# Optimization experiments

Hardware: AMD Instinct MI355X
Metric: run time of the kernel (lower is better)

The kernel has to match this reference:

```python
import jax, jax.numpy as jnp
import numpy as np

B = 4096          # batch_size
D = 256           # embedding dim
N = 2 * B
TEMPERATURE = 0.5
GAMMA = 2.0
ALPHA = 0.25


def _negative_indices():
    # Static column indices of negatives per row: all columns except self (i)
    # and the positive partner ((i+B) mod N). Shape (N, N-2).
    idx = []
    for i in range(N):
        partner = (i + B) % N
        cols = [j for j in range(N) if j != i and j != partner]
        idx.append(cols)
    return np.asarray(idx, dtype=np.int32)

_NEG_IDX = jnp.asarray(_negative_indices())


def setup_inputs() -> dict:
    key = jax.random.key(0)
    kx, ky = jax.random.split(key)
    zx = jax.random.normal(kx, (B, D), dtype=jnp.float32)
    zy = jax.random.normal(ky, (B, D), dtype=jnp.float32)
    return {"zx": zx, "zy": zy}


def reference(zx, zy):
    z = jnp.concatenate([zx, zy], axis=0)                    # (N, D)
    zn = z / jnp.linalg.norm(z, axis=1, keepdims=True)       # cosine normalize
    sim = (zn @ zn.T) / TEMPERATURE                          # (N, N)

    sim_xy = jnp.diagonal(sim, offset=B)                     # (B,)
    sim_yx = jnp.diagonal(sim, offset=-B)                    # (B,)
    pos = jnp.concatenate([sim_xy, sim_yx])[:, None]         # (N, 1)
    neg = jnp.take_along_axis(sim, _NEG_IDX, axis=1)         # (N, N-2)

    logits = jnp.concatenate([pos, neg], axis=1)             # (N, N-1)
    # CE with label 0 for every row: -log_softmax(logits)[:, 0]
    ce = jax.nn.logsumexp(logits, axis=1) - logits[:, 0]
    pt = jnp.exp(-ce)
    focal = (1.0 - pt) ** GAMMA * ce
    return (ALPHA * focal).mean()
```

## Files before the change

kernel.cpp:

```cpp
#include <hip/hip_runtime.h>
#include <stdint.h>
#include <stddef.h>


typedef __attribute__((ext_vector_type(8))) short short8;
typedef __attribute__((ext_vector_type(4))) float f32x4;

#define NROWS 8192
#define DDIM 256
#define NTILES 2080
#define NBLK 512

__device__ __forceinline__ unsigned short f2bf(float f) {
  unsigned int u = __float_as_uint(f);
  u = (u + 0x7FFFu + ((u >> 16) & 1u)) >> 16;
  return (unsigned short)u;
}

__device__ __forceinline__ void unrank_tile(int t, int& p_out, int& q_out) {
  int p = (int)((129.0f - sqrtf((float)(16641 - 8 * t))) * 0.5f);
  p = max(0, min(63, p));
  while ((((p + 1) * (129 - (p + 1))) >> 1) <= t) ++p;
  while (((p * (129 - p)) >> 1) > t) --p;
  p_out = p;
  q_out = p + (t - ((p * (129 - p)) >> 1));
}

__global__ __launch_bounds__(256) void norm_kernel(const float* __restrict__ zx,
                                                   const float* __restrict__ zy,
                                                   unsigned short* __restrict__ zn,
                                                   unsigned int* __restrict__ counter) {
  if (blockIdx.x == 0 && threadIdx.x == 0) *counter = 0u;
  const int row = blockIdx.x * 4 + (threadIdx.x >> 6);
  const int lane = threadIdx.x & 63;
  const float* src = (row < 4096) ? (zx + (size_t)row * DDIM)
                                  : (zy + (size_t)(row - 4096) * DDIM);
  float4 v = reinterpret_cast<const float4*>(src)[lane];
  float ss = v.x * v.x + v.y * v.y + v.z * v.z + v.w * v.w;
#pragma unroll
  for (int m = 1; m < 64; m <<= 1) ss += __shfl_xor(ss, m);
  const float sc = 1.69864360f * rsqrtf(ss);
  ushort4 o;
  o.x = f2bf(v.x * sc); o.y = f2bf(v.y * sc);
  o.z = f2bf(v.z * sc); o.w = f2bf(v.w * sc);
  reinterpret_cast<ushort4*>(zn + (size_t)row * DDIM)[lane] = o;
}

__global__ __launch_bounds__(256, 2) void simtri_kernel(const unsigned short* __restrict__ zn,
                                                        float* __restrict__ partial,
                                                        float* __restrict__ pos) {
  __shared__ unsigned short smem[2][2][128 * 64];
  const int bid = blockIdx.x;
  const int nt = (bid < NTILES - NBLK * 4) ? 5 : 4;
  const int tid = threadIdx.x;
  const int lane = tid & 63;
  const int wid = tid >> 6;
  const int wr = wid >> 1;
  const int wc = wid & 1;

  const f32x4 z4 = {0.f, 0.f, 0.f, 0.f};
  f32x4 acc[4][4];
#pragma unroll
  for (int m = 0; m < 4; ++m)
#pragma unroll
    for (int n = 0; n < 4; ++n) acc[m][n] = z4;

  auto stage_one = [&](int buf, int which, int row0, int k0) {
    unsigned short* lb = &smem[buf][which][0];
#pragma unroll
    for (int j = 0; j < 4; ++j) {
      const int u = j * 256 + wid * 64 + lane;
      const unsigned short* g = zn + (size_t)(row0 + (u >> 3)) * DDIM + k0 + (u & 7) * 8;
      unsigned short* l = lb + (size_t)(j * 256 + wid * 64) * 8;
      __builtin_amdgcn_global_load_lds(
          (const __attribute__((address_space(1))) void*)g,
          (__attribute__((address_space(3))) void*)l, 16, 0, 0);
    }
  };
  auto stageT = [&](int buf, int p, int q, int k0) {
    stage_one(buf, 0, p << 7, k0);
    if (p != q) stage_one(buf, 1, q << 7, k0);
  };

  int cp, cq;
  unrank_tile(bid, cp, cq);
  stageT(0, cp, cq, 0);
  __syncthreads();

  int buf = 0;
  for (int i = 0; i < nt; ++i) {
    int np = cp, nq = cq;
    const bool have_next = (i + 1 < nt);
    if (have_next) unrank_tile(bid + NBLK * (i + 1), np, nq);
    const bool isdiag = (cp == cq);
    const bool ispos = (cq == cp + 32);
    const int R0 = cp << 7;
    const int C0 = cq << 7;

#pragma unroll
    for (int kk = 0; kk < 4; ++kk) {
      if (kk < 3) stageT(buf ^ 1, cp, cq, (kk + 1) * 64);
      else if (have_next) stageT(buf ^ 1, np, nq, 0);
      const unsigned short* A = &smem[buf][0][0];
      const unsigned short* Bm = isdiag ? A : &smem[buf][1][0];
#pragma unroll
      for (int ks = 0; ks < 2; ++ks) {
        short8 af[4], bfr[4];
#pragma unroll
        for (int m = 0; m < 4; ++m)
          af[m] = *reinterpret_cast<const short8*>(
              A + ((wr * 64 + m * 16 + (lane & 15)) * 64 + ks * 32 + (lane >> 4) * 8));
#pragma unroll
        for (int n = 0; n < 4; ++n)
          bfr[n] = *reinterpret_cast<const short8*>(
              Bm + ((wc * 64 + n * 16 + (lane & 15)) * 64 + ks * 32 + (lane >> 4) * 8));
#pragma unroll
        for (int m = 0; m < 4; ++m)
#pragma unroll
          for (int n = 0; n < 4; ++n)
            acc[m][n] = __builtin_amdgcn_mfma_f32_16x16x32_bf16(af[m], bfr[n], acc[m][n], 0, 0, 0);
      }
      buf ^= 1;
      if (kk < 3) __syncthreads();
    }

    float rsum[4][4];
    float csum[4];
#pragma unroll
    for (int m = 0; m < 4; ++m)
#pragma unroll
      for (int r = 0; r < 4; ++r) rsum[m][r] = 0.f;
#pragma unroll
    for (int n = 0; n < 4; ++n) csum[n] = 0.f;

#pragma unroll
    for (int m = 0; m < 4; ++m)
#pragma unroll
      for (int n = 0; n < 4; ++n)
#pragma unroll
        for (int r = 0; r < 4; ++r) {
          const float e = __builtin_amdgcn_exp2f(acc[m][n][r]);
          rsum[m][r] += e;
          csum[n] += e;
        }

    if ((isdiag || ispos) && (wr == wc)) {
      const int hi = lane >> 4, lo = lane & 15;
#pragma unroll
      for (int m = 0; m < 4; ++m)
#pragma unroll
        for (int r = 0; r < 4; ++r)
          if (lo == 4 * hi + r) {
            if (isdiag) rsum[m][r] -= __builtin_amdgcn_exp2f(acc[m][m][r]);
            else        pos[R0 + wr * 64 + m * 16 + lo] = acc[m][m][r];
          }
    }

#pragma unroll
    for (int m = 0; m < 4; ++m)
#pragma unroll
      for (int r = 0; r < 4; ++r) {
        float s = rsum[m][r];
        s += __shfl_xor(s, 1); s += __shfl_xor(s, 2);
        s += __shfl_xor(s, 4); s += __shfl_xor(s, 8);
        if ((lane & 15) == 0) {
          const int grow = R0 + wr * 64 + m * 16 + ((lane >> 4) << 2) + r;
          partial[(size_t)(cq * 2 + wc) * NROWS + grow] = s;
        }
      }

    if (!isdiag) {
#pragma unroll
      for (int n = 0; n < 4; ++n) {
        float c = csum[n];
        c += __shfl_xor(c, 16); c += __shfl_xor(c, 32);
        if (lane < 16)
          partial[(size_t)(cp * 2 + wr) * NROWS + (C0 + wc * 64 + n * 16 + lane)] = c;
      }
    }

#pragma unroll
    for (int m = 0; m < 4; ++m)
#pragma unroll
      for (int n = 0; n < 4; ++n) acc[m][n] = z4;

    __syncthreads();
    cp = np; cq = nq;
  }
}

__global__ __launch_bounds__(256) void d1_kernel(const float* __restrict__ partial,
                                                 const float* __restrict__ pos,
                                                 float* __restrict__ bsum,
                                                 float* __restrict__ out,
                                                 unsigned int* __restrict__ counter) {
  const int row = blockIdx.x * 256 + threadIdx.x;
  float s = 0.f;
#pragma unroll 16
  for (int c = 0; c < 128; ++c) s += partial[(size_t)c * NROWS + row];
  const float L = __log2f(s) - pos[row & 4095];
  const float pt = __builtin_amdgcn_exp2f(-L);
  const float ce = 0.69314718056f * L;
  float f = (1.f - pt) * (1.f - pt) * ce;
#pragma unroll
  for (int m = 1; m < 64; m <<= 1) f += __shfl_xor(f, m);
  __shared__ float wsum[4];
  if ((threadIdx.x & 63) == 0) wsum[threadIdx.x >> 6] = f;
  __syncthreads();
  if (threadIdx.x == 0) {
    bsum[blockIdx.x] = wsum[0] + wsum[1] + wsum[2] + wsum[3];
    __threadfence();
    if (atomicAdd(counter, 1u) == 31u) {
      __threadfence();
      float v = 0.f;
#pragma unroll
      for (int c = 0; c < 32; ++c) v += ((const volatile float*)bsum)[c];
      out[0] = 0.25f * v / 8192.f;
    }
  }
}

extern "C" void kernel_launch(void* const* d_in, const int* in_sizes, int n_in,
                              void* d_out, int out_size, void* d_ws, size_t ws_size,
                              hipStream_t stream) {
  const float* zx = (const float*)d_in[0];
  const float* zy = (const float*)d_in[1];
  float* out = (float*)d_out;

  unsigned short* zn = (unsigned short*)d_ws;
  float* pos = (float*)((char*)d_ws + (size_t)NROWS * DDIM * 2);
  float* partial = pos + 4096;
  float* bsum = partial + (size_t)128 * NROWS;
  unsigned int* counter = (unsigned int*)(bsum + 32);

  norm_kernel<<<2048, 256, 0, stream>>>(zx, zy, zn, counter);
  simtri_kernel<<<NBLK, 256, 0, stream>>>(zn, partial, pos);
  d1_kernel<<<32, 256, 0, stream>>>(partial, pos, bsum, out, counter);
}
```

Before: 110.2 us.

## Swizzle LDS layout and assign contiguous tile runs per block with XCD remap

```diff
diff --git a/kernel.cpp b/kernel.cpp
--- a/kernel.cpp
+++ b/kernel.cpp
@@ -50,13 +50,18 @@
                                                         float* __restrict__ partial,
                                                         float* __restrict__ pos) {
   __shared__ unsigned short smem[2][2][128 * 64];
-  const int bid = blockIdx.x;
-  const int nt = (bid < NTILES - NBLK * 4) ? 5 : 4;
+  const int c = (blockIdx.x & 7) * 64 + (blockIdx.x >> 3);
+  int start, nt;
+  if (c < 32) { start = c * 5;              nt = 5; }
+  else        { start = 160 + (c - 32) * 4; nt = 4; }
+
   const int tid = threadIdx.x;
   const int lane = tid & 63;
   const int wid = tid >> 6;
   const int wr = wid >> 1;
   const int wc = wid & 1;
+  const int hi = lane >> 4, lo = lane & 15;
+  const int sw = lo & 7;
 
   const f32x4 z4 = {0.f, 0.f, 0.f, 0.f};
   f32x4 acc[4][4];
@@ -69,8 +74,10 @@
     unsigned short* lb = &smem[buf][which][0];
 #pragma unroll
     for (int j = 0; j < 4; ++j) {
-      const int u = j * 256 + wid * 64 + lane;
-      const unsigned short* g = zn + (size_t)(row0 + (u >> 3)) * DDIM + k0 + (u & 7) * 8;
+      const int u = j * 256 + tid;
+      const int r = u >> 3, ul = u & 7;
+      const unsigned short* g =
+          zn + (size_t)(row0 + r) * DDIM + k0 + ((ul ^ (r & 7)) << 3);
       unsigned short* l = lb + (size_t)(j * 256 + wid * 64) * 8;
       __builtin_amdgcn_global_load_lds(
           (const __attribute__((address_space(1))) void*)g,
@@ -83,7 +90,7 @@
   };
 
   int cp, cq;
-  unrank_tile(bid, cp, cq);
+  unrank_tile(start, cp, cq);
   stageT(0, cp, cq, 0);
   __syncthreads();
 
@@ -91,7 +98,7 @@
   for (int i = 0; i < nt; ++i) {
     int np = cp, nq = cq;
     const bool have_next = (i + 1 < nt);
-    if (have_next) unrank_tile(bid + NBLK * (i + 1), np, nq);
+    if (have_next) { if (cq == 63) { np = cp + 1; nq = np; } else { nq = cq + 1; } }
     const bool isdiag = (cp == cq);
     const bool ispos = (cq == cp + 32);
     const int R0 = cp << 7;
@@ -109,11 +116,11 @@
 #pragma unroll
         for (int m = 0; m < 4; ++m)
           af[m] = *reinterpret_cast<const short8*>(
-              A + ((wr * 64 + m * 16 + (lane & 15)) * 64 + ks * 32 + (lane >> 4) * 8));
+              A + ((wr * 64 + m * 16 + lo) * 64 + (((ks * 4 + hi) ^ sw) << 3)));
 #pragma unroll
         for (int n = 0; n < 4; ++n)
           bfr[n] = *reinterpret_cast<const short8*>(
-              Bm + ((wc * 64 + n * 16 + (lane & 15)) * 64 + ks * 32 + (lane >> 4) * 8));
+              Bm + ((wc * 64 + n * 16 + lo) * 64 + (((ks * 4 + hi) ^ sw) << 3)));
 #pragma unroll
         for (int m = 0; m < 4; ++m)
 #pragma unroll
@@ -145,7 +152,6 @@
         }
 
     if ((isdiag || ispos) && (wr == wc)) {
-      const int hi = lane >> 4, lo = lane & 15;
 #pragma unroll
       for (int m = 0; m < 4; ++m)
 #pragma unroll
@@ -163,8 +169,8 @@
         float s = rsum[m][r];
         s += __shfl_xor(s, 1); s += __shfl_xor(s, 2);
         s += __shfl_xor(s, 4); s += __shfl_xor(s, 8);
-        if ((lane & 15) == 0) {
-          const int grow = R0 + wr * 64 + m * 16 + ((lane >> 4) << 2) + r;
+        if (lo == 0) {
+          const int grow = R0 + wr * 64 + m * 16 + (hi << 2) + r;
           partial[(size_t)(cq * 2 + wc) * NROWS + grow] = s;
         }
       }
@@ -172,10 +178,10 @@
     if (!isdiag) {
 #pragma unroll
       for (int n = 0; n < 4; ++n) {
-        float c = csum[n];
-        c += __shfl_xor(c, 16); c += __shfl_xor(c, 32);
+        float cs = csum[n];
+        cs += __shfl_xor(cs, 16); cs += __shfl_xor(cs, 32);
         if (lane < 16)
-          partial[(size_t)(cp * 2 + wr) * NROWS + (C0 + wc * 64 + n * 16 + lane)] = c;
+          partial[(size_t)(cp * 2 + wr) * NROWS + (C0 + wc * 64 + n * 16 + lane)] = cs;
       }
     }
 
```

Result: faster. 104.9 us (-4.8%).
